# Kernel tuning notes

Measured on AMD Instinct MI355X. Metric: run time of the kernel, lower is better.

## Reference

```python
import jax, jax.numpy as jnp
import numpy as np

H = 8  # num_heads, fixed in the module


def setup_inputs() -> dict:
    key = jax.random.key(0)
    ks = jax.random.split(key, 26)
    C = 256          # hidden_dim
    K = 16           # num_corners
    B = 8            # images
    P = 64           # proposals per image
    N = B * P        # total proposals
    Hf = Wf = 14     # feature map HxW (T = 196 keys per proposal)
    Hq = Wq = 10     # query grid (S = 100 queries)
    s = 1.0 / np.sqrt(C)

    def w(k, shape):
        return jax.random.normal(k, shape, jnp.float32) * s

    return {
        "features": jax.random.normal(ks[0], (N, C, Hf, Wf), jnp.float32),
        "query_features": jax.random.normal(ks[1], (B, C, Hq, Wq), jnp.float32),
        # self-attention params (torch MHA: y = x @ W.T + b)
        "wq_s": w(ks[2], (C, C)), "wk_s": w(ks[3], (C, C)), "wv_s": w(ks[4], (C, C)),
        "bq_s": jnp.zeros((C,), jnp.float32), "bk_s": jnp.zeros((C,), jnp.float32), "bv_s": jnp.zeros((C,), jnp.float32),
        "wo_s": w(ks[5], (C, C)), "bo_s": jnp.zeros((C,), jnp.float32),
        # cross-attention params
        "wq_c": w(ks[6], (C, C)), "wk_c": w(ks[7], (C, C)), "wv_c": w(ks[8], (C, C)),
        "bq_c": jnp.zeros((C,), jnp.float32), "bk_c": jnp.zeros((C,), jnp.float32), "bv_c": jnp.zeros((C,), jnp.float32),
        "wo_c": w(ks[9], (C, C)), "bo_c": jnp.zeros((C,), jnp.float32),
        # polygon MLP head
        "w1": w(ks[10], (C, C)), "b1": jnp.zeros((C,), jnp.float32),
        "w2": w(ks[11], (2 * K, C)), "b2": jnp.zeros((2 * K,), jnp.float32),
        # score head
        "ws": w(ks[12], (1, C)), "bs": jnp.zeros((1,), jnp.float32),
    }


def _forward(features, query_features,
             wq_s, wk_s, wv_s, bq_s, bk_s, bv_s, wo_s, bo_s,
             wq_c, wk_c, wv_c, bq_c, bk_c, bv_c, wo_c, bo_c,
             w1, b1, w2, b2, ws, bs):
    B, C = query_features.shape[0], query_features.shape[1]
    dh = C // H
    scale = 1.0 / jnp.sqrt(jnp.asarray(dh, jnp.float32))

    # query_features: (B,C,Hq,Wq) -> (S,B,C)
    qf = query_features.reshape(B, C, -1).transpose(2, 0, 1)
    S = qf.shape[0]

    # ---- self-attention over queries ----
    q = (qf @ wq_s.T + bq_s).reshape(S, B, H, dh)
    k = (qf @ wk_s.T + bk_s).reshape(S, B, H, dh)
    v = (qf @ wv_s.T + bv_s).reshape(S, B, H, dh)
    att = jax.nn.softmax(jnp.einsum('sbhd,tbhd->bhst', q, k) * scale, axis=-1)
    qsa = jnp.einsum('bhst,tbhd->sbhd', att, v).reshape(S, B, C) @ wo_s.T + bo_s  # (S,B,C)

    # features: (N,C,Hf,Wf) -> (B,P,T,C) with T=Hf*Wf, P=N//B
    N = features.shape[0]
    P = N // B
    feats = features.reshape(N, C, -1).transpose(0, 2, 1).reshape(B, P, -1, C)

    # ---- cross-attention: same (S,C) query broadcast over P proposals ----
    qc = (qsa @ wq_c.T + bq_c).reshape(S, B, H, dh)
    kc = (feats @ wk_c.T + bk_c).reshape(B, P, -1, H, dh)
    vc = (feats @ wv_c.T + bv_c).reshape(B, P, -1, H, dh)
    sc = jnp.einsum('sbhd,bpthd->bphst', qc, kc) * scale  # (B,P,H,S,T)
    a = jax.nn.softmax(sc, axis=-1)
    o = jnp.einsum('bphst,bpthd->bpshd', a, vc).reshape(B, P, S, C) @ wo_c.T + bo_c  # (B,P,S,C)

    # ---- heads, then mean over the S query positions ----
    h1 = jax.nn.relu(o @ w1.T + b1)
    polygons = (h1 @ w2.T + b2).mean(axis=2).reshape(N, -1)          # (N, 2K)
    scores = jax.nn.sigmoid(o @ ws.T + bs).mean(axis=2).reshape(N, 1)  # (N, 1)
    return polygons, scores


def reference(features, query_features,
              wq_s, wk_s, wv_s, bq_s, bk_s, bv_s, wo_s, bo_s,
              wq_c, wk_c, wv_c, bq_c, bk_c, bv_c, wo_c, bo_c,
              w1, b1, w2, b2, ws, bs):
    return _forward(features, query_features,
                    wq_s, wk_s, wv_s, bq_s, bk_s, bv_s, wo_s, bo_s,
                    wq_c, wk_c, wv_c, bq_c, bk_c, bv_c, wo_c, bo_c,
                    w1, b1, w2, b2, ws, bs)
```

## Files before the change

kernel.cpp:

```cpp
#include <hip/hip_runtime.h>
#include <hip/hip_bf16.h>


typedef __attribute__((ext_vector_type(8))) short bf16x8;
typedef __attribute__((ext_vector_type(4))) float f32x4;

__device__ __forceinline__ float bf2f(ushort u) {
    union { float f; uint u32; } v; v.u32 = ((uint)u) << 16; return v.f;
}
__device__ __forceinline__ ushort f2bf(float f) {
    union { float f; uint u; } v; v.f = f;
    uint r = v.u + 0x7FFF + ((v.u >> 16) & 1);
    return (ushort)(r >> 16);
}
__device__ __forceinline__ uint pk2(float a, float b) {
    __hip_bfloat162 h = __float22bfloat162_rn(make_float2(a, b));
    union { __hip_bfloat162 h2; uint u; } c; c.h2 = h; return c.u;
}
__device__ __forceinline__ f32x4 MFMA(bf16x8 a, bf16x8 b, f32x4 c) {
    return __builtin_amdgcn_mfma_f32_16x16x32_bf16(a, b, c, 0, 0, 0);
}

#define SCALE_DH 0.17677669529663687f

#define TOTALW (2337 * 256)
#define QCPN   (8 * 8 * 112 * 32)
#define NBIAS  2337

__global__ void prep_kernel(const float* w0, const float* w1_, const float* w2_,
                            const float* w3, const float* w4, const float* w5,
                            const float* w6, const float* w7, const float* w8,
                            const float* w9, const float* w10,
                            const float* b0, const float* b1_, const float* b2_,
                            const float* b3, const float* b4, const float* b5,
                            const float* b6, const float* b7, const float* b8,
                            const float* b9, const float* b10,
                            ushort* wbf, float* bias, ushort* qcp)
{
    for (size_t i = blockIdx.x * blockDim.x + threadIdx.x;
         i < (size_t)TOTALW + QCPN + NBIAS; i += (size_t)gridDim.x * blockDim.x) {
        if (i < TOTALW) {
            int row = (int)(i >> 8), col = (int)(i & 255);
            const float* sp; int base;
            if      (row < 256)  { sp = w0;  base = 0; }
            else if (row < 512)  { sp = w1_; base = 256; }
            else if (row < 768)  { sp = w2_; base = 512; }
            else if (row < 1024) { sp = w3;  base = 768; }
            else if (row < 1280) { sp = w4;  base = 1024; }
            else if (row < 1536) { sp = w5;  base = 1280; }
            else if (row < 1792) { sp = w6;  base = 1536; }
            else if (row < 2048) { sp = w7;  base = 1792; }
            else if (row < 2304) { sp = w8;  base = 2048; }
            else if (row < 2336) { sp = w9;  base = 2304; }
            else                 { sp = w10; base = 2336; }
            wbf[i] = f2bf(sp[(size_t)(row - base) * 256 + col]);
        } else if (i < (size_t)TOTALW + QCPN) {
            qcp[i - TOTALW] = 0;
        } else {
            int idx = (int)(i - TOTALW - QCPN);
            const float* sp; int base;
            if      (idx < 256)  { sp = b0;  base = 0; }
            else if (idx < 512)  { sp = b1_; base = 256; }
            else if (idx < 768)  { sp = b2_; base = 512; }
            else if (idx < 1024) { sp = b3;  base = 768; }
            else if (idx < 1280) { sp = b4;  base = 1024; }
            else if (idx < 1536) { sp = b5;  base = 1280; }
            else if (idx < 1792) { sp = b6;  base = 1536; }
            else if (idx < 2048) { sp = b7;  base = 1792; }
            else if (idx < 2304) { sp = b8;  base = 2048; }
            else if (idx < 2336) { sp = b9;  base = 2304; }
            else                 { sp = b10; base = 2336; }
            bias[idx] = sp[idx - base];
        }
    }
}

template<int ASRC, int GS, int EPI>
__global__ __launch_bounds__(256)
void gemm_rows(const void* Aptr, const ushort* Wall, const float* Ball,
               ushort* Out, int M, int Wrow0, int Brow0, int ldo)
{
    __shared__ ushort As[64 * 40];
    __shared__ ushort Bs[128 * 40];
    int tid = threadIdx.x;
    int lane = tid & 63, w = tid >> 6;
    int lr = lane & 15, lg = lane >> 4;
    int r0 = blockIdx.x * 64;
    int j0 = blockIdx.y * 128;

    f32x4 acc[4][2];
    #pragma unroll
    for (int mt = 0; mt < 4; ++mt)
        #pragma unroll
        for (int nt = 0; nt < 2; ++nt) { f32x4 z = {0.f,0.f,0.f,0.f}; acc[mt][nt] = z; }

    for (int ks = 0; ks < 8; ++ks) {
        int c0 = ks * 32;
        {
            int i = tid >> 2, q = tid & 3;
            int r = r0 + i;
            if (ASRC == 0) {
                uint4 v = make_uint4(0u,0u,0u,0u);
                if (r < M) v = *(const uint4*)((const ushort*)Aptr + (size_t)r * 256 + c0 + q * 8);
                *(uint4*)(&As[i * 40 + q * 8]) = v;
            } else {
                uint u[4] = {0u,0u,0u,0u};
                if (r < M) {
                    int g = r / GS, o = r - g * GS;
                    const float* src = (const float*)Aptr + (size_t)g * 256 * GS + o;
                    #pragma unroll
                    for (int k2 = 0; k2 < 4; ++k2) {
                        ushort a0 = f2bf(src[(size_t)(c0 + q * 8 + 2 * k2)     * GS]);
                        ushort a1 = f2bf(src[(size_t)(c0 + q * 8 + 2 * k2 + 1) * GS]);
                        u[k2] = (uint)a0 | ((uint)a1 << 16);
                    }
                }
                *(uint4*)(&As[i * 40 + q * 8]) = make_uint4(u[0], u[1], u[2], u[3]);
            }
        }
        {
            int jj = tid >> 1, half = tid & 1;
            const ushort* src = Wall + (size_t)(Wrow0 + j0 + jj) * 256 + c0 + half * 16;
            ushort* dst = &Bs[jj * 40 + half * 16];
            *(uint4*)(dst)     = *(const uint4*)(src);
            *(uint4*)(dst + 8) = *(const uint4*)(src + 8);
        }
        __syncthreads();
        bf16x8 bfr[2];
        #pragma unroll
        for (int nt = 0; nt < 2; ++nt)
            bfr[nt] = *(const bf16x8*)(&Bs[(w * 32 + nt * 16 + lr) * 40 + lg * 8]);
        #pragma unroll
        for (int mt = 0; mt < 4; ++mt) {
            bf16x8 afr = *(const bf16x8*)(&As[(mt * 16 + lr) * 40 + lg * 8]);
            acc[mt][0] = MFMA(afr, bfr[0], acc[mt][0]);
            acc[mt][1] = MFMA(afr, bfr[1], acc[mt][1]);
        }
        __syncthreads();
    }
    #pragma unroll
    for (int mt = 0; mt < 4; ++mt) {
        #pragma unroll
        for (int nt = 0; nt < 2; ++nt) {
            int jc = j0 + w * 32 + nt * 16 + lr;
            float bias = Ball[Brow0 + jc];
            #pragma unroll
            for (int rg = 0; rg < 4; ++rg) {
                int r = r0 + mt * 16 + lg * 4 + rg;
                if (r >= M) continue;
                float vv = acc[mt][nt][rg] + bias;
                if (EPI == 0) {
                    Out[(size_t)r * ldo + jc] = f2bf(vv);
                } else {
                    int b = r / 100, s = r - b * 100;
                    int h = jc >> 5, d = jc & 31;
                    Out[(((size_t)(b * 8 + h)) * 112 + s) * 32 + d] = f2bf(vv * SCALE_DH);
                }
            }
        }
    }
}

__global__ __launch_bounds__(128)
void self_attn(const ushort* qkv, ushort* sav)
{
    __shared__ float kls[100][33];
    __shared__ float vls[100][33];
    __shared__ float sls[100][101];
    int bh = blockIdx.x; int b = bh >> 3, h = bh & 7;
    int tid = threadIdx.x;
    for (int idx = tid; idx < 100 * 32; idx += 128) {
        int t = idx >> 5, d = idx & 31;
        kls[t][d] = bf2f(qkv[((size_t)(b * 100 + t)) * 768 + 256 + h * 32 + d]);
        vls[t][d] = bf2f(qkv[((size_t)(b * 100 + t)) * 768 + 512 + h * 32 + d]);
    }
    __syncthreads();
    if (tid < 100) {
        int s = tid;
        float q[32];
        #pragma unroll
        for (int d = 0; d < 32; ++d)
            q[d] = bf2f(qkv[((size_t)(b * 100 + s)) * 768 + h * 32 + d]) * SCALE_DH;
        float mx = -1e30f;
        for (int t = 0; t < 100; ++t) {
            float sc = 0.f;
            #pragma unroll
            for (int d = 0; d < 32; ++d) sc += q[d] * kls[t][d];
            sls[s][t] = sc; mx = fmaxf(mx, sc);
        }
        float sum = 0.f;
        for (int t = 0; t < 100; ++t) {
            float p = __expf(sls[s][t] - mx);
            sls[s][t] = p; sum += p;
        }
        float inv = 1.f / sum;
        float acc2[32];
        #pragma unroll
        for (int d = 0; d < 32; ++d) acc2[d] = 0.f;
        for (int t = 0; t < 100; ++t) {
            float pv = sls[s][t];
            #pragma unroll
            for (int d = 0; d < 32; ++d) acc2[d] += pv * vls[t][d];
        }
        #pragma unroll
        for (int d = 0; d < 32; ++d)
            sav[((size_t)(b * 100 + s)) * 256 + h * 32 + d] = f2bf(acc2[d] * inv);
    }
}

__global__ __launch_bounds__(512, 2)
void kvproj(const float* features, const ushort* Wall, const float* Ball,
            ushort* kc, ushort* vc, int n_base)
{
    __shared__ ushort featT[224 * 264];
    int tid = threadIdx.x;
    int lane = tid & 63, w = tid >> 6;
    int lr = lane & 15, lg = lane >> 4;
    int nl = blockIdx.x;
    int n  = n_base + nl;
    const float* fb = features + (size_t)n * 256 * 196;

    bf16x8 af[4][8];
    #pragma unroll
    for (int m = 0; m < 4; ++m) {
        int row = ((m < 2) ? 1280 : 1536) + w * 32 + (m & 1) * 16 + lr;
        #pragma unroll
        for (int ks = 0; ks < 8; ++ks)
            af[m][ks] = *(const bf16x8*)(Wall + (size_t)row * 256 + ks * 32 + lg * 8);
    }
    float biask0 = Ball[1280 + w * 32 + lr];
    float biask1 = Ball[1296 + w * 32 + lr];
    float biasv0 = Ball[1536 + w * 32 + lr];
    float biasv1 = Ball[1552 + w * 32 + lr];

    #pragma unroll
    for (int it = 0; it < 7; ++it) {
        int idx = tid + it * 512;
        if (idx < 3136) {
            int cg = idx / 49, tq = idx - cg * 49;
            const float* p = fb + (size_t)(cg * 4) * 196 + tq * 4;
            float4 v0 = *(const float4*)(p);
            float4 v1 = *(const float4*)(p + 196);
            float4 v2 = *(const float4*)(p + 392);
            float4 v3 = *(const float4*)(p + 588);
            #pragma unroll
            for (int j = 0; j < 4; ++j) {
                float e0 = (j == 0) ? v0.x : (j == 1) ? v0.y : (j == 2) ? v0.z : v0.w;
                float e1 = (j == 0) ? v1.x : (j == 1) ? v1.y : (j == 2) ? v1.z : v1.w;
                float e2 = (j == 0) ? v2.x : (j == 1) ? v2.y : (j == 2) ? v2.z : v2.w;
                float e3 = (j == 0) ? v3.x : (j == 1) ? v3.y : (j == 2) ? v3.z : v3.w;
                uint2 pr;
                pr.x = pk2(e0, e1);
                pr.y = pk2(e2, e3);
                *(uint2*)(&featT[(tq * 4 + j) * 264 + cg * 4]) = pr;
            }
        }
    }
    for (int idx = tid; idx < 12 * 264; idx += 512)
        featT[196 * 264 + idx] = 0;
    __syncthreads();

    for (int tt = 0; tt < 13; ++tt) {
        bf16x8 a8[8];
        #pragma unroll
        for (int ks = 0; ks < 8; ++ks)
            a8[ks] = *(const bf16x8*)(&featT[(tt * 16 + lr) * 264 + ks * 32 + lg * 8]);
        f32x4 acc[4];
        #pragma unroll
        for (int m = 0; m < 4; ++m) { f32x4 z = {0.f,0.f,0.f,0.f}; acc[m] = z; }
        #pragma unroll
        for (int ks = 0; ks < 8; ++ks)
            #pragma unroll
            for (int m = 0; m < 4; ++m)
                acc[m] = MFMA(a8[ks], af[m][ks], acc[m]);

        int tb = tt * 16 + lg * 4;
        #pragma unroll
        for (int rg = 0; rg < 4; ++rg) {
            int t = tb + rg;
            if (t < 196) {
                kc[((size_t)nl * 224 + t) * 256 + w * 32 + lr]      = f2bf(acc[0][rg] + biask0);
                kc[((size_t)nl * 224 + t) * 256 + w * 32 + 16 + lr] = f2bf(acc[1][rg] + biask1);
            }
        }
        if (tb < 196) {
            size_t vb0 = ((size_t)nl * 256 + w * 32 + lr) * 224 + tb;
            size_t vb1 = ((size_t)nl * 256 + w * 32 + 16 + lr) * 224 + tb;
            uint a01 = pk2(acc[2][0] + biasv0, acc[2][1] + biasv0);
            uint a23 = pk2(acc[2][2] + biasv0, acc[2][3] + biasv0);
            uint b01 = pk2(acc[3][0] + biasv1, acc[3][1] + biasv1);
            uint b23 = pk2(acc[3][2] + biasv1, acc[3][3] + biasv1);
            *(uint*)(vc + vb0)     = a01;
            *(uint*)(vc + vb0 + 2) = a23;
            *(uint*)(vc + vb1)     = b01;
            *(uint*)(vc + vb1 + 2) = b23;
        }
    }
}

__global__ __launch_bounds__(512, 2)
void attn_fuse(const ushort* qcp, const ushort* kc, const ushort* vc,
               const ushort* Wall, const float* Ball, float* outp, int n_base)
{
    __shared__ char smem[130816];
    ushort* OL  = (ushort*)smem;
    float* hbar = (float*)(smem + 59392);
    float* scb  = (float*)(smem + 60416);
    ushort* O2  = (ushort*)(smem + 71680);

    int tid = threadIdx.x;
    int lane = tid & 63; int w = tid >> 6;
    int lr = lane & 15, lg = lane >> 4;
    int nl = blockIdx.x; int n = n_base + nl;
    int b = n >> 6;
    const ushort* kcn = kc + (size_t)nl * 224 * 256;
    const ushort* vcn = vc + (size_t)nl * 256 * 224;

    bf16x8 qf[7];
    #pragma unroll
    for (int mt = 0; mt < 7; ++mt)
        qf[mt] = *(const bf16x8*)(qcp + ((((size_t)(b * 8 + w)) * 112 + mt * 16 + lr) * 32 + lg * 8));

    bf16x8 ones;
    #pragma unroll
    for (int j = 0; j < 8; ++j) ones[j] = (short)0x3F80;

    f32x4 o_acc[7][2], l_acc[7];
    #pragma unroll
    for (int mt = 0; mt < 7; ++mt) {
        f32x4 z = {0.f,0.f,0.f,0.f};
        o_acc[mt][0] = z; o_acc[mt][1] = z; l_acc[mt] = z;
    }

    const ushort* kbase = kcn + (size_t)lr * 256 + w * 32 + lg * 8;
    const ushort* vb0 = vcn + ((size_t)(w * 32 + lr)) * 224;
    const ushort* vb1 = vcn + ((size_t)(w * 32 + 16 + lr)) * 224;

    bf16x8 ck0, ck1;
    uint2 v0lo, v0hi, v1lo, v1hi;
    ck0 = *(const bf16x8*)(kbase);
    ck1 = *(const bf16x8*)(kbase + 16 * 256);
    v0lo = *(const uint2*)(vb0 + 4 * lg);
    v0hi = *(const uint2*)(vb0 + 16 + 4 * lg);
    v1lo = *(const uint2*)(vb1 + 4 * lg);
    v1hi = *(const uint2*)(vb1 + 16 + 4 * lg);

    for (int ch = 0; ch < 7; ++ch) {
        int t0 = ch * 32;
        bf16x8 nk0, nk1;
        uint2 n0lo, n0hi, n1lo, n1hi;
        if (ch < 6) {
            int t0n = t0 + 32;
            nk0 = *(const bf16x8*)(kbase + (size_t)t0n * 256);
            nk1 = *(const bf16x8*)(kbase + (size_t)(t0n + 16) * 256);
            n0lo = *(const uint2*)(vb0 + t0n + 4 * lg);
            n0hi = *(const uint2*)(vb0 + t0n + 16 + 4 * lg);
            n1lo = *(const uint2*)(vb1 + t0n + 4 * lg);
            n1hi = *(const uint2*)(vb1 + t0n + 16 + 4 * lg);
            if (t0n == 192) {
                uint2 zz = make_uint2(0u, 0u);
                n0hi = zz; n1hi = zz;
                if (lg) { n0lo = zz; n1lo = zz; }
            }
        }
        union { uint4 q; bf16x8 v; } u0, u1;
        u0.q = make_uint4(v0lo.x, v0lo.y, v0hi.x, v0hi.y);
        u1.q = make_uint4(v1lo.x, v1lo.y, v1hi.x, v1hi.y);
        bool mA[4], mB[4];
        #pragma unroll
        for (int r = 0; r < 4; ++r) {
            mA[r] = (t0 + 4 * lg + r)      >= 196;
            mB[r] = (t0 + 16 + 4 * lg + r) >= 196;
        }
        #pragma unroll
        for (int mt = 0; mt < 7; ++mt) {
            f32x4 z = {0.f,0.f,0.f,0.f};
            f32x4 s0 = MFMA(ck0, qf[mt], z);
            f32x4 s1 = MFMA(ck1, qf[mt], z);
            float p00 = mA[0] ? 0.f : __expf(s0[0]);
            float p01 = mA[1] ? 0.f : __expf(s0[1]);
            float p02 = mA[2] ? 0.f : __expf(s0[2]);
            float p03 = mA[3] ? 0.f : __expf(s0[3]);
            float p10 = mB[0] ? 0.f : __expf(s1[0]);
            float p11 = mB[1] ? 0.f : __expf(s1[1]);
            float p12 = mB[2] ? 0.f : __expf(s1[2]);
            float p13 = mB[3] ? 0.f : __expf(s1[3]);
            union { uint4 q; bf16x8 v; } pu;
            pu.q.x = pk2(p00, p01);
            pu.q.y = pk2(p02, p03);
            pu.q.z = pk2(p10, p11);
            pu.q.w = pk2(p12, p13);
            o_acc[mt][0] = MFMA(pu.v, u0.v, o_acc[mt][0]);
            o_acc[mt][1] = MFMA(pu.v, u1.v, o_acc[mt][1]);
            l_acc[mt]    = MFMA(pu.v, ones, l_acc[mt]);
        }
        ck0 = nk0; ck1 = nk1;
        v0lo = n0lo; v0hi = n0hi; v1lo = n1lo; v1hi = n1hi;
    }

    #pragma unroll
    for (int mt = 0; mt < 7; ++mt) {
        #pragma unroll
        for (int r = 0; r < 4; ++r) {
            float inv = 1.f / l_acc[mt][r];
            int srow = mt * 16 + lg * 4 + r;
            OL[srow * 264 + w * 32 + lr]      = f2bf(o_acc[mt][0][r] * inv);
            OL[srow * 264 + w * 32 + 16 + lr] = f2bf(o_acc[mt][1][r] * inv);
        }
    }
    __syncthreads();

    {
        f32x4 a2[7][2];
        #pragma unroll
        for (int mt = 0; mt < 7; ++mt)
            #pragma unroll
            for (int nt = 0; nt < 2; ++nt) { f32x4 z = {0.f,0.f,0.f,0.f}; a2[mt][nt] = z; }
        for (int ks = 0; ks < 8; ++ks) {
            int c0 = ks * 32;
            bf16x8 bw[2];
            #pragma unroll
            for (int nt = 0; nt < 2; ++nt)
                bw[nt] = *(const bf16x8*)(Wall + (size_t)(1792 + w * 32 + nt * 16 + lr) * 256 + c0 + lg * 8);
            #pragma unroll
            for (int mt = 0; mt < 7; ++mt) {
                bf16x8 af = *(const bf16x8*)(&OL[(mt * 16 + lr) * 264 + c0 + lg * 8]);
                a2[mt][0] = MFMA(af, bw[0], a2[mt][0]);
                a2[mt][1] = MFMA(af, bw[1], a2[mt][1]);
            }
        }
        #pragma unroll
        for (int mt = 0; mt < 7; ++mt)
            #pragma unroll
            for (int nt = 0; nt < 2; ++nt) {
                float bias = Ball[1792 + w * 32 + nt * 16 + lr];
                #pragma unroll
                for (int r = 0; r < 4; ++r) {
                    int srow = mt * 16 + lg * 4 + r;
                    O2[srow * 264 + w * 32 + nt * 16 + lr] = f2bf(a2[mt][nt][r] + bias);
                }
            }
    }
    __syncthreads();

    {
        f32x4 a2[7][2];
        #pragma unroll
        for (int mt = 0; mt < 7; ++mt)
            #pragma unroll
            for (int nt = 0; nt < 2; ++nt) { f32x4 z = {0.f,0.f,0.f,0.f}; a2[mt][nt] = z; }
        for (int ks = 0; ks < 8; ++ks) {
            int c0 = ks * 32;
            bf16x8 bw[2];
            #pragma unroll
            for (int nt = 0; nt < 2; ++nt)
                bw[nt] = *(const bf16x8*)(Wall + (size_t)(2048 + w * 32 + nt * 16 + lr) * 256 + c0 + lg * 8);
            #pragma unroll
            for (int mt = 0; mt < 7; ++mt) {
                bf16x8 af = *(const bf16x8*)(&O2[(mt * 16 + lr) * 264 + c0 + lg * 8]);
                a2[mt][0] = MFMA(af, bw[0], a2[mt][0]);
                a2[mt][1] = MFMA(af, bw[1], a2[mt][1]);
            }
        }
        __syncthreads();
        #pragma unroll
        for (int mt = 0; mt < 7; ++mt)
            #pragma unroll
            for (int nt = 0; nt < 2; ++nt) {
                float bias = Ball[2048 + w * 32 + nt * 16 + lr];
                #pragma unroll
                for (int r = 0; r < 4; ++r) {
                    int srow = mt * 16 + lg * 4 + r;
                    float v = a2[mt][nt][r] + bias;
                    v = v > 0.f ? v : 0.f;
                    OL[srow * 264 + w * 32 + nt * 16 + lr] = f2bf(v);
                }
            }
    }
    __syncthreads();

    if (tid < 256) {
        float s = 0.f;
        for (int srow = 0; srow < 100; ++srow) s += bf2f(OL[srow * 264 + tid]);
        hbar[tid] = s * 0.01f;
    }
    if (tid < 100) {
        float s = 0.f;
        for (int c2 = 0; c2 < 256; ++c2)
            s += bf2f(O2[tid * 264 + c2]) * bf2f(Wall[(size_t)2336 * 256 + c2]);
        s += Ball[2336];
        scb[tid] = 1.f / (1.f + __expf(-s));
    }
    __syncthreads();
    if (tid < 32) {
        float s = 0.f;
        for (int c2 = 0; c2 < 256; ++c2)
            s += hbar[c2] * bf2f(Wall[(size_t)(2304 + tid) * 256 + c2]);
        s += Ball[2304 + tid];
        outp[(size_t)n * 32 + tid] = s;
    }
    if (tid == 64) {
        float s = 0.f;
        for (int i2 = 0; i2 < 100; ++i2) s += scb[i2];
        outp[16384 + n] = s * 0.01f;
    }
}

extern "C" void kernel_launch(void* const* d_in, const int* in_sizes, int n_in,
                              void* d_out, int out_size, void* d_ws, size_t ws_size,
                              hipStream_t stream)
{
    const float* features = (const float*)d_in[0];
    const float* qfeat    = (const float*)d_in[1];
    char* ws = (char*)d_ws;

    ushort* wbf  = (ushort*)ws;
    float*  bias = (float*)(ws + 1196544);
    ushort* qkv  = (ushort*)(ws + 1206016);
    ushort* sav  = (ushort*)(ws + 2434816);
    ushort* osb  = (ushort*)(ws + 2844416);
    ushort* qcp  = (ushort*)(ws + 3254016);
    ushort* kvb  = (ushort*)(ws + 3712768);

    prep_kernel<<<dim3(512), dim3(256), 0, stream>>>(
        (const float*)d_in[2], (const float*)d_in[3], (const float*)d_in[4],
        (const float*)d_in[8], (const float*)d_in[10], (const float*)d_in[11],
        (const float*)d_in[12], (const float*)d_in[16], (const float*)d_in[18],
        (const float*)d_in[20], (const float*)d_in[22],
        (const float*)d_in[5], (const float*)d_in[6], (const float*)d_in[7],
        (const float*)d_in[9], (const float*)d_in[13], (const float*)d_in[14],
        (const float*)d_in[15], (const float*)d_in[17], (const float*)d_in[19],
        (const float*)d_in[21], (const float*)d_in[23],
        wbf, bias, qcp);

    gemm_rows<1, 100, 0><<<dim3(13, 6), dim3(256), 0, stream>>>(
        qfeat, wbf, bias, qkv, 800, 0, 0, 768);
    self_attn<<<dim3(64), dim3(128), 0, stream>>>(qkv, sav);
    gemm_rows<0, 1, 0><<<dim3(13, 2), dim3(256), 0, stream>>>(
        sav, wbf, bias, osb, 800, 768, 768, 256);
    gemm_rows<0, 1, 1><<<dim3(13, 2), dim3(256), 0, stream>>>(
        osb, wbf, bias, qcp, 800, 1024, 1024, 0);

    const size_t per_n = 229376;
    long avail = (long)ws_size - 3712768L;
    int Np = 512;
    if (avail < (long)(per_n * 512)) {
        Np = (int)(avail / (long)per_n);
        if (Np < 1) Np = 1;
    }
    ushort* kcb = kvb;
    ushort* vcb = kvb + (size_t)Np * 224 * 256;
    float* outp = (float*)d_out;
    for (int n0 = 0; n0 < 512; n0 += Np) {
        int cnt = (512 - n0 < Np) ? (512 - n0) : Np;
        kvproj<<<dim3(cnt), dim3(512), 0, stream>>>(features, wbf, bias, kcb, vcb, n0);
        attn_fuse<<<dim3(cnt), dim3(512), 0, stream>>>(qcp, kcb, vcb, wbf, bias, outp, n0);
    }
}
```

Before: 206.8 us.

## Split kvproj and attn_fuse work across 16 waves and shrink LDS usage

kvproj now runs 1024-thread blocks on a 2D grid that splits the 196 keys into two halves, with separate waves computing K and V, which halves per-block LDS and register tiles. attn_fuse uses 16 waves that split the query row tiles into two groups per head. It also reuses a single LDS buffer for the attention output, the out-projection and the MLP hidden, with extra barriers, and overlaps the score-head reduction with the second GEMM. The goal is more waves per CU and less LDS per block. The cost is duplicated weight-fragment loads and more synchronisation.

```diff
diff --git a/kernel.cpp b/kernel.cpp
--- a/kernel.cpp
+++ b/kernel.cpp
@@ -208,41 +208,48 @@
     }
 }
 
-__global__ __launch_bounds__(512, 2)
+__global__ __launch_bounds__(1024, 4)
 void kvproj(const float* features, const ushort* Wall, const float* Ball,
             ushort* kc, ushort* vc, int n_base)
 {
-    __shared__ ushort featT[224 * 264];
+    __shared__ ushort featT[112 * 264];
     int tid = threadIdx.x;
     int lane = tid & 63, w = tid >> 6;
     int lr = lane & 15, lg = lane >> 4;
     int nl = blockIdx.x;
     int n  = n_base + nl;
+    int th = blockIdx.y;
+    int t0b = th * 112;
     const float* fb = features + (size_t)n * 256 * 196;
 
-    bf16x8 af[4][8];
-    #pragma unroll
-    for (int m = 0; m < 4; ++m) {
-        int row = ((m < 2) ? 1280 : 1536) + w * 32 + (m & 1) * 16 + lr;
+    bool isV = (w >= 8);
+    int g = isV ? (w - 8) : w;
+    int wrow0 = (isV ? 1536 : 1280) + g * 32;
+
+    bf16x8 af[2][8];
+    #pragma unroll
+    for (int m = 0; m < 2; ++m)
         #pragma unroll
         for (int ks = 0; ks < 8; ++ks)
-            af[m][ks] = *(const bf16x8*)(Wall + (size_t)row * 256 + ks * 32 + lg * 8);
-    }
-    float biask0 = Ball[1280 + w * 32 + lr];
-    float biask1 = Ball[1296 + w * 32 + lr];
-    float biasv0 = Ball[1536 + w * 32 + lr];
-    float biasv1 = Ball[1552 + w * 32 + lr];
-
-    #pragma unroll
-    for (int it = 0; it < 7; ++it) {
-        int idx = tid + it * 512;
-        if (idx < 3136) {
-            int cg = idx / 49, tq = idx - cg * 49;
-            const float* p = fb + (size_t)(cg * 4) * 196 + tq * 4;
-            float4 v0 = *(const float4*)(p);
-            float4 v1 = *(const float4*)(p + 196);
-            float4 v2 = *(const float4*)(p + 392);
-            float4 v3 = *(const float4*)(p + 588);
+            af[m][ks] = *(const bf16x8*)(Wall + (size_t)(wrow0 + m * 16 + lr) * 256 + ks * 32 + lg * 8);
+    float bias0 = Ball[wrow0 + lr];
+    float bias1 = Ball[wrow0 + 16 + lr];
+
+    #pragma unroll
+    for (int it = 0; it < 2; ++it) {
+        int idx = tid + it * 1024;
+        if (idx < 1792) {
+            int cg = idx / 28, tq = idx - cg * 28;
+            int t = t0b + tq * 4;
+            float4 z4 = {0.f, 0.f, 0.f, 0.f};
+            float4 v0 = z4, v1 = z4, v2 = z4, v3 = z4;
+            if (t < 196) {
+                const float* p = fb + (size_t)(cg * 4) * 196 + t;
+                v0 = *(const float4*)(p);
+                v1 = *(const float4*)(p + 196);
+                v2 = *(const float4*)(p + 392);
+                v3 = *(const float4*)(p + 588);
+            }
             #pragma unroll
             for (int j = 0; j < 4; ++j) {
                 float e0 = (j == 0) ? v0.x : (j == 1) ? v0.y : (j == 2) ? v0.z : v0.w;
@@ -256,40 +263,34 @@
             }
         }
     }
-    for (int idx = tid; idx < 12 * 264; idx += 512)
-        featT[196 * 264 + idx] = 0;
-    __syncthreads();
-
-    for (int tt = 0; tt < 13; ++tt) {
-        bf16x8 a8[8];
-        #pragma unroll
-        for (int ks = 0; ks < 8; ++ks)
-            a8[ks] = *(const bf16x8*)(&featT[(tt * 16 + lr) * 264 + ks * 32 + lg * 8]);
-        f32x4 acc[4];
-        #pragma unroll
-        for (int m = 0; m < 4; ++m) { f32x4 z = {0.f,0.f,0.f,0.f}; acc[m] = z; }
-        #pragma unroll
-        for (int ks = 0; ks < 8; ++ks)
+    __syncthreads();
+
+    int ttmax = th ? 6 : 7;
+    for (int tt = 0; tt < ttmax; ++tt) {
+        f32x4 acc0 = {0.f,0.f,0.f,0.f}, acc1 = {0.f,0.f,0.f,0.f};
+        #pragma unroll
+        for (int ks = 0; ks < 8; ++ks) {
+            bf16x8 a = *(const bf16x8*)(&featT[(tt * 16 + lr) * 264 + ks * 32 + lg * 8]);
+            acc0 = MFMA(a, af[0][ks], acc0);
+            acc1 = MFMA(a, af[1][ks], acc1);
+        }
+        int tb = t0b + tt * 16 + lg * 4;
+        if (!isV) {
             #pragma unroll
-            for (int m = 0; m < 4; ++m)
-                acc[m] = MFMA(a8[ks], af[m][ks], acc[m]);
-
-        int tb = tt * 16 + lg * 4;
-        #pragma unroll
-        for (int rg = 0; rg < 4; ++rg) {
-            int t = tb + rg;
-            if (t < 196) {
-                kc[((size_t)nl * 224 + t) * 256 + w * 32 + lr]      = f2bf(acc[0][rg] + biask0);
-                kc[((size_t)nl * 224 + t) * 256 + w * 32 + 16 + lr] = f2bf(acc[1][rg] + biask1);
-            }
-        }
-        if (tb < 196) {
-            size_t vb0 = ((size_t)nl * 256 + w * 32 + lr) * 224 + tb;
-            size_t vb1 = ((size_t)nl * 256 + w * 32 + 16 + lr) * 224 + tb;
-            uint a01 = pk2(acc[2][0] + biasv0, acc[2][1] + biasv0);
-            uint a23 = pk2(acc[2][2] + biasv0, acc[2][3] + biasv0);
-            uint b01 = pk2(acc[3][0] + biasv1, acc[3][1] + biasv1);
-            uint b23 = pk2(acc[3][2] + biasv1, acc[3][3] + biasv1);
+            for (int rg = 0; rg < 4; ++rg) {
+                int t = tb + rg;
+                if (t < 196) {
+                    kc[((size_t)nl * 224 + t) * 256 + g * 32 + lr]      = f2bf(acc0[rg] + bias0);
+                    kc[((size_t)nl * 224 + t) * 256 + g * 32 + 16 + lr] = f2bf(acc1[rg] + bias1);
+                }
+            }
+        } else if (tb < 196) {
+            size_t vb0 = ((size_t)nl * 256 + g * 32 + lr) * 224 + tb;
+            size_t vb1 = ((size_t)nl * 256 + g * 32 + 16 + lr) * 224 + tb;
+            uint a01 = pk2(acc0[0] + bias0, acc0[1] + bias0);
+            uint a23 = pk2(acc0[2] + bias0, acc0[3] + bias0);
+            uint b01 = pk2(acc1[0] + bias1, acc1[1] + bias1);
+            uint b23 = pk2(acc1[2] + bias1, acc1[3] + bias1);
             *(uint*)(vc + vb0)     = a01;
             *(uint*)(vc + vb0 + 2) = a23;
             *(uint*)(vc + vb1)     = b01;
@@ -298,43 +299,45 @@
     }
 }
 
-__global__ __launch_bounds__(512, 2)
+__global__ __launch_bounds__(1024, 4)
 void attn_fuse(const ushort* qcp, const ushort* kc, const ushort* vc,
                const ushort* Wall, const float* Ball, float* outp, int n_base)
 {
-    __shared__ char smem[130816];
-    ushort* OL  = (ushort*)smem;
+    __shared__ char smem[60816];
+    ushort* OB  = (ushort*)smem;
     float* hbar = (float*)(smem + 59392);
     float* scb  = (float*)(smem + 60416);
-    ushort* O2  = (ushort*)(smem + 71680);
 
     int tid = threadIdx.x;
-    int lane = tid & 63; int w = tid >> 6;
+    int lane = tid & 63; int wv = tid >> 6;
+    int h = wv & 7, sh = wv >> 3;
+    int mt0 = sh * 4, mtn = sh ? 3 : 4;
     int lr = lane & 15, lg = lane >> 4;
     int nl = blockIdx.x; int n = n_base + nl;
     int b = n >> 6;
     const ushort* kcn = kc + (size_t)nl * 224 * 256;
     const ushort* vcn = vc + (size_t)nl * 256 * 224;
 
-    bf16x8 qf[7];
-    #pragma unroll
-    for (int mt = 0; mt < 7; ++mt)
-        qf[mt] = *(const bf16x8*)(qcp + ((((size_t)(b * 8 + w)) * 112 + mt * 16 + lr) * 32 + lg * 8));
+    bf16x8 qf[4];
+    #pragma unroll
+    for (int mti = 0; mti < 4; ++mti)
+        if (mti < mtn)
+            qf[mti] = *(const bf16x8*)(qcp + ((((size_t)(b * 8 + h)) * 112 + (mt0 + mti) * 16 + lr) * 32 + lg * 8));
 
     bf16x8 ones;
     #pragma unroll
     for (int j = 0; j < 8; ++j) ones[j] = (short)0x3F80;
 
-    f32x4 o_acc[7][2], l_acc[7];
-    #pragma unroll
-    for (int mt = 0; mt < 7; ++mt) {
+    f32x4 o_acc[4][2], l_acc[4];
+    #pragma unroll
+    for (int mti = 0; mti < 4; ++mti) {
         f32x4 z = {0.f,0.f,0.f,0.f};
-        o_acc[mt][0] = z; o_acc[mt][1] = z; l_acc[mt] = z;
-    }
-
-    const ushort* kbase = kcn + (size_t)lr * 256 + w * 32 + lg * 8;
-    const ushort* vb0 = vcn + ((size_t)(w * 32 + lr)) * 224;
-    const ushort* vb1 = vcn + ((size_t)(w * 32 + 16 + lr)) * 224;
+        o_acc[mti][0] = z; o_acc[mti][1] = z; l_acc[mti] = z;
+    }
+
+    const ushort* kbase = kcn + (size_t)lr * 256 + h * 32 + lg * 8;
+    const ushort* vb0 = vcn + ((size_t)(h * 32 + lr)) * 224;
+    const ushort* vb1 = vcn + ((size_t)(h * 32 + 16 + lr)) * 224;
 
     bf16x8 ck0, ck1;
     uint2 v0lo, v0hi, v1lo, v1hi;
@@ -373,123 +376,135 @@
             mB[r] = (t0 + 16 + 4 * lg + r) >= 196;
         }
         #pragma unroll
-        for (int mt = 0; mt < 7; ++mt) {
-            f32x4 z = {0.f,0.f,0.f,0.f};
-            f32x4 s0 = MFMA(ck0, qf[mt], z);
-            f32x4 s1 = MFMA(ck1, qf[mt], z);
-            float p00 = mA[0] ? 0.f : __expf(s0[0]);
-            float p01 = mA[1] ? 0.f : __expf(s0[1]);
-            float p02 = mA[2] ? 0.f : __expf(s0[2]);
-            float p03 = mA[3] ? 0.f : __expf(s0[3]);
-            float p10 = mB[0] ? 0.f : __expf(s1[0]);
-            float p11 = mB[1] ? 0.f : __expf(s1[1]);
-            float p12 = mB[2] ? 0.f : __expf(s1[2]);
-            float p13 = mB[3] ? 0.f : __expf(s1[3]);
-            union { uint4 q; bf16x8 v; } pu;
-            pu.q.x = pk2(p00, p01);
-            pu.q.y = pk2(p02, p03);
-            pu.q.z = pk2(p10, p11);
-            pu.q.w = pk2(p12, p13);
-            o_acc[mt][0] = MFMA(pu.v, u0.v, o_acc[mt][0]);
-            o_acc[mt][1] = MFMA(pu.v, u1.v, o_acc[mt][1]);
-            l_acc[mt]    = MFMA(pu.v, ones, l_acc[mt]);
+        for (int mti = 0; mti < 4; ++mti) {
+            if (mti < mtn) {
+                f32x4 z = {0.f,0.f,0.f,0.f};
+                f32x4 s0 = MFMA(ck0, qf[mti], z);
+                f32x4 s1 = MFMA(ck1, qf[mti], z);
+                float p00 = mA[0] ? 0.f : __expf(s0[0]);
+                float p01 = mA[1] ? 0.f : __expf(s0[1]);
+                float p02 = mA[2] ? 0.f : __expf(s0[2]);
+                float p03 = mA[3] ? 0.f : __expf(s0[3]);
+                float p10 = mB[0] ? 0.f : __expf(s1[0]);
+                float p11 = mB[1] ? 0.f : __expf(s1[1]);
+                float p12 = mB[2] ? 0.f : __expf(s1[2]);
+                float p13 = mB[3] ? 0.f : __expf(s1[3]);
+                union { uint4 q; bf16x8 v; } pu;
+                pu.q.x = pk2(p00, p01);
+                pu.q.y = pk2(p02, p03);
+                pu.q.z = pk2(p10, p11);
+                pu.q.w = pk2(p12, p13);
+                o_acc[mti][0] = MFMA(pu.v, u0.v, o_acc[mti][0]);
+                o_acc[mti][1] = MFMA(pu.v, u1.v, o_acc[mti][1]);
+                l_acc[mti]    = MFMA(pu.v, ones, l_acc[mti]);
+            }
         }
         ck0 = nk0; ck1 = nk1;
         v0lo = n0lo; v0hi = n0hi; v1lo = n1lo; v1hi = n1hi;
     }
 
     #pragma unroll
-    for (int mt = 0; mt < 7; ++mt) {
-        #pragma unroll
-        for (int r = 0; r < 4; ++r) {
-            float inv = 1.f / l_acc[mt][r];
-            int srow = mt * 16 + lg * 4 + r;
-            OL[srow * 264 + w * 32 + lr]      = f2bf(o_acc[mt][0][r] * inv);
-            OL[srow * 264 + w * 32 + 16 + lr] = f2bf(o_acc[mt][1][r] * inv);
+    for (int mti = 0; mti < 4; ++mti) {
+        if (mti < mtn) {
+            #pragma unroll
+            for (int r = 0; r < 4; ++r) {
+                float inv = 1.f / l_acc[mti][r];
+                int srow = (mt0 + mti) * 16 + lg * 4 + r;
+                OB[srow * 264 + h * 32 + lr]      = f2bf(o_acc[mti][0][r] * inv);
+                OB[srow * 264 + h * 32 + 16 + lr] = f2bf(o_acc[mti][1][r] * inv);
+            }
+        }
+    }
+    __syncthreads();
+
+    f32x4 a2[4][2];
+    #pragma unroll
+    for (int mti = 0; mti < 4; ++mti) {
+        f32x4 z = {0.f,0.f,0.f,0.f}; a2[mti][0] = z; a2[mti][1] = z;
+    }
+    for (int ks = 0; ks < 8; ++ks) {
+        int c0 = ks * 32;
+        bf16x8 bw0 = *(const bf16x8*)(Wall + (size_t)(1792 + h * 32 + lr) * 256 + c0 + lg * 8);
+        bf16x8 bw1 = *(const bf16x8*)(Wall + (size_t)(1792 + h * 32 + 16 + lr) * 256 + c0 + lg * 8);
+        #pragma unroll
+        for (int mti = 0; mti < 4; ++mti) {
+            if (mti < mtn) {
+                bf16x8 afr = *(const bf16x8*)(&OB[((mt0 + mti) * 16 + lr) * 264 + c0 + lg * 8]);
+                a2[mti][0] = MFMA(afr, bw0, a2[mti][0]);
+                a2[mti][1] = MFMA(afr, bw1, a2[mti][1]);
+            }
         }
     }
     __syncthreads();
 
     {
-        f32x4 a2[7][2];
-        #pragma unroll
-        for (int mt = 0; mt < 7; ++mt)
-            #pragma unroll
-            for (int nt = 0; nt < 2; ++nt) { f32x4 z = {0.f,0.f,0.f,0.f}; a2[mt][nt] = z; }
-        for (int ks = 0; ks < 8; ++ks) {
-            int c0 = ks * 32;
-            bf16x8 bw[2];
-            #pragma unroll
-            for (int nt = 0; nt < 2; ++nt)
-                bw[nt] = *(const bf16x8*)(Wall + (size_t)(1792 + w * 32 + nt * 16 + lr) * 256 + c0 + lg * 8);
-            #pragma unroll
-            for (int mt = 0; mt < 7; ++mt) {
-                bf16x8 af = *(const bf16x8*)(&OL[(mt * 16 + lr) * 264 + c0 + lg * 8]);
-                a2[mt][0] = MFMA(af, bw[0], a2[mt][0]);
-                a2[mt][1] = MFMA(af, bw[1], a2[mt][1]);
-            }
-        }
-        #pragma unroll
-        for (int mt = 0; mt < 7; ++mt)
-            #pragma unroll
-            for (int nt = 0; nt < 2; ++nt) {
-                float bias = Ball[1792 + w * 32 + nt * 16 + lr];
+        float biasA = Ball[1792 + h * 32 + lr];
+        float biasB = Ball[1792 + h * 32 + 16 + lr];
+        #pragma unroll
+        for (int mti = 0; mti < 4; ++mti) {
+            if (mti < mtn) {
                 #pragma unroll
                 for (int r = 0; r < 4; ++r) {
-                    int srow = mt * 16 + lg * 4 + r;
-                    O2[srow * 264 + w * 32 + nt * 16 + lr] = f2bf(a2[mt][nt][r] + bias);
+                    int srow = (mt0 + mti) * 16 + lg * 4 + r;
+                    OB[srow * 264 + h * 32 + lr]      = f2bf(a2[mti][0][r] + biasA);
+                    OB[srow * 264 + h * 32 + 16 + lr] = f2bf(a2[mti][1][r] + biasB);
                 }
             }
-    }
-    __syncthreads();
-
-    {
-        f32x4 a2[7][2];
-        #pragma unroll
-        for (int mt = 0; mt < 7; ++mt)
-            #pragma unroll
-            for (int nt = 0; nt < 2; ++nt) { f32x4 z = {0.f,0.f,0.f,0.f}; a2[mt][nt] = z; }
-        for (int ks = 0; ks < 8; ++ks) {
-            int c0 = ks * 32;
-            bf16x8 bw[2];
-            #pragma unroll
-            for (int nt = 0; nt < 2; ++nt)
-                bw[nt] = *(const bf16x8*)(Wall + (size_t)(2048 + w * 32 + nt * 16 + lr) * 256 + c0 + lg * 8);
-            #pragma unroll
-            for (int mt = 0; mt < 7; ++mt) {
-                bf16x8 af = *(const bf16x8*)(&O2[(mt * 16 + lr) * 264 + c0 + lg * 8]);
-                a2[mt][0] = MFMA(af, bw[0], a2[mt][0]);
-                a2[mt][1] = MFMA(af, bw[1], a2[mt][1]);
-            }
-        }
-        __syncthreads();
-        #pragma unroll
-        for (int mt = 0; mt < 7; ++mt)
-            #pragma unroll
-            for (int nt = 0; nt < 2; ++nt) {
-                float bias = Ball[2048 + w * 32 + nt * 16 + lr];
-                #pragma unroll
-                for (int r = 0; r < 4; ++r) {
-                    int srow = mt * 16 + lg * 4 + r;
-                    float v = a2[mt][nt][r] + bias;
-                    v = v > 0.f ? v : 0.f;
-                    OL[srow * 264 + w * 32 + nt * 16 + lr] = f2bf(v);
-                }
-            }
-    }
-    __syncthreads();
-
-    if (tid < 256) {
-        float s = 0.f;
-        for (int srow = 0; srow < 100; ++srow) s += bf2f(OL[srow * 264 + tid]);
-        hbar[tid] = s * 0.01f;
+        }
+    }
+    __syncthreads();
+
+    #pragma unroll
+    for (int mti = 0; mti < 4; ++mti) {
+        f32x4 z = {0.f,0.f,0.f,0.f}; a2[mti][0] = z; a2[mti][1] = z;
+    }
+    for (int ks = 0; ks < 8; ++ks) {
+        int c0 = ks * 32;
+        bf16x8 bw0 = *(const bf16x8*)(Wall + (size_t)(2048 + h * 32 + lr) * 256 + c0 + lg * 8);
+        bf16x8 bw1 = *(const bf16x8*)(Wall + (size_t)(2048 + h * 32 + 16 + lr) * 256 + c0 + lg * 8);
+        #pragma unroll
+        for (int mti = 0; mti < 4; ++mti) {
+            if (mti < mtn) {
+                bf16x8 afr = *(const bf16x8*)(&OB[((mt0 + mti) * 16 + lr) * 264 + c0 + lg * 8]);
+                a2[mti][0] = MFMA(afr, bw0, a2[mti][0]);
+                a2[mti][1] = MFMA(afr, bw1, a2[mti][1]);
+            }
+        }
     }
     if (tid < 100) {
         float s = 0.f;
         for (int c2 = 0; c2 < 256; ++c2)
-            s += bf2f(O2[tid * 264 + c2]) * bf2f(Wall[(size_t)2336 * 256 + c2]);
+            s += bf2f(OB[tid * 264 + c2]) * bf2f(Wall[(size_t)2336 * 256 + c2]);
         s += Ball[2336];
         scb[tid] = 1.f / (1.f + __expf(-s));
+    }
+    __syncthreads();
+
+    {
+        float biasA = Ball[2048 + h * 32 + lr];
+        float biasB = Ball[2048 + h * 32 + 16 + lr];
+        #pragma unroll
+        for (int mti = 0; mti < 4; ++mti) {
+            if (mti < mtn) {
+                #pragma unroll
+                for (int r = 0; r < 4; ++r) {
+                    int srow = (mt0 + mti) * 16 + lg * 4 + r;
+                    float vA = a2[mti][0][r] + biasA;
+                    float vB = a2[mti][1][r] + biasB;
+                    vA = vA > 0.f ? vA : 0.f;
+                    vB = vB > 0.f ? vB : 0.f;
+                    OB[srow * 264 + h * 32 + lr]      = f2bf(vA);
+                    OB[srow * 264 + h * 32 + 16 + lr] = f2bf(vB);
+                }
+            }
+        }
+    }
+    __syncthreads();
+
+    if (tid < 256) {
+        float s = 0.f;
+        for (int srow = 0; srow < 100; ++srow) s += bf2f(OB[srow * 264 + tid]);
+        hbar[tid] = s * 0.01f;
     }
     __syncthreads();
     if (tid < 32) {
@@ -553,7 +568,7 @@
     float* outp = (float*)d_out;
     for (int n0 = 0; n0 < 512; n0 += Np) {
         int cnt = (512 - n0 < Np) ? (512 - n0) : Np;
-        kvproj<<<dim3(cnt), dim3(512), 0, stream>>>(features, wbf, bias, kcb, vcb, n0);
-        attn_fuse<<<dim3(cnt), dim3(512), 0, stream>>>(qcp, kcb, vcb, wbf, bias, outp, n0);
-    }
-}
+        kvproj<<<dim3(cnt, 2), dim3(1024), 0, stream>>>(features, wbf, bias, kcb, vcb, n0);
+        attn_fuse<<<dim3(cnt), dim3(1024), 0, stream>>>(qcp, kcb, vcb, wbf, bias, outp, n0);
+    }
+}
```

Measured after the change: 244.3 us. 18.2% more time.
